# Kernel tuning notes

Measured on AMD Instinct MI355X. Metric: run time of the kernel, lower is better.

## Reference

```python
import jax, jax.numpy as jnp
import numpy as np

RADIUS = 0.1
NSAMPLE = 32


def setup_inputs() -> dict:
    key = jax.random.key(0)
    k1, k2, k3, k4, k5 = jax.random.split(key, 5)
    B, NPOINT, N, C = 4, 2048, 8192, 64
    query_xyz = jax.random.uniform(k1, (B, 3, NPOINT), dtype=jnp.float32)
    support_xyz = jax.random.uniform(k2, (B, 3, N), dtype=jnp.float32)
    query_mask = jax.random.bernoulli(k3, 0.9, (B, NPOINT))
    support_mask = jax.random.bernoulli(k4, 0.9, (B, N))
    features = jax.random.normal(k5, (B, C, N), dtype=jnp.float32)
    return {"query_xyz": query_xyz, "support_xyz": support_xyz,
            "query_mask": query_mask, "support_mask": support_mask,
            "features": features}


def _masked_ordered_ball_query(query_xyz, support_xyz, query_mask, support_mask,
                               radius, nsample):
    # query_xyz: (B,3,npoint), support_xyz: (B,3,N)
    q = query_xyz.transpose(0, 2, 1)    # (B, npoint, 3)
    s = support_xyz.transpose(0, 2, 1)  # (B, N, 3)
    N = s.shape[1]
    # squared pairwise distances via |q|^2 + |s|^2 - 2 q.s  -> (B, npoint, N)
    d2 = (jnp.sum(q * q, -1)[:, :, None]
          + jnp.sum(s * s, -1)[:, None, :]
          - 2.0 * jnp.einsum('bpd,bnd->bpn', q, s))
    within = (d2 <= radius * radius) \
        & support_mask[:, None, :] & query_mask[:, :, None]
    # ordered selection of the first `nsample` in-ball indices (ascending index)
    score = jnp.where(within, N - jnp.arange(N, dtype=jnp.int32), 0)
    vals, idx = jax.lax.top_k(score, nsample)     # (B, npoint, nsample)
    idx_mask = vals > 0                            # true neighbors
    # pad slots with the first found neighbor (0 if none found)
    first = jnp.where(idx_mask[..., :1], idx[..., :1], 0)
    idx = jnp.where(idx_mask, idx, first)
    return idx, idx_mask


def _group(points_nc, idx):
    # points_nc: (B, N, D), idx: (B, npoint, nsample) -> (B, npoint, nsample, D)
    return jax.vmap(lambda p, i: p[i])(points_nc, idx)


def reference(query_xyz, support_xyz, query_mask, support_mask, features):
    idx, idx_mask = _masked_ordered_ball_query(
        query_xyz, support_xyz, query_mask, support_mask, RADIUS, NSAMPLE)
    s = support_xyz.transpose(0, 2, 1)             # (B, N, 3)
    grouped_xyz = _group(s, idx).transpose(0, 3, 1, 2)   # (B,3,npoint,nsample)
    grouped_xyz = grouped_xyz - query_xyz[:, :, :, None]
    grouped_xyz = grouped_xyz / RADIUS             # normalize_xyz=True
    f = features.transpose(0, 2, 1)                # (B, N, C)
    grouped_features = _group(f, idx).transpose(0, 3, 1, 2)  # (B,C,npoint,nsample)
    new_features = jnp.concatenate([grouped_xyz, grouped_features], axis=1)
    return new_features, idx_mask
```

## Files before the change

kernel.cpp:

```cpp
#include <hip/hip_runtime.h>


#define NPOINT 2048
#define NSUP   8192
#define NCH    64
#define NS     32
#define GRID1  10
#define CELLS  1000
#define QCHUNK 1024

__device__ __forceinline__ bool probe_mask4(const void* mask) {
    const unsigned char* mb = (const unsigned char*)mask;
    const int lane = threadIdx.x & 63;
    return __ballot(mb[4 * lane + 1] != 0) == 0ull;
}
__device__ __forceinline__ bool read_mask(const void* mask, int i, bool is4) {
    return is4 ? (((const int*)mask)[i] != 0)
               : (((const unsigned char*)mask)[i] != 0);
}
__device__ __forceinline__ int cell_of(float x, float y, float z) {
    const int cx = min(GRID1 - 1, (int)(x * 10.0f));
    const int cy = min(GRID1 - 1, (int)(y * 10.0f));
    const int cz = min(GRID1 - 1, (int)(z * 10.0f));
    return cx + GRID1 * cy + GRID1 * GRID1 * cz;
}

__global__ __launch_bounds__(1024) void build_grid(
    const float* __restrict__ support_xyz, const void* __restrict__ support_mask,
    int* __restrict__ starts, float4* __restrict__ pts)
{
    __shared__ int hist[CELLS];
    __shared__ int scanb[1024];
    __shared__ int cur[CELLS];
    const int b   = blockIdx.x;
    const int tid = threadIdx.x;
    const bool m4 = probe_mask4(support_mask);
    const float* sx = support_xyz + (size_t)b * 3 * NSUP;

    if (tid < CELLS) { hist[tid] = 0; cur[tid] = 0; }
    __syncthreads();

    float xr[8], yr[8], zr[8]; int cidr[8]; bool mr[8];
    #pragma unroll
    for (int i = 0; i < 8; ++i) {
        const int n = tid + 1024 * i;
        xr[i] = sx[n];
        yr[i] = sx[NSUP + n];
        zr[i] = sx[2 * NSUP + n];
        mr[i] = read_mask(support_mask, b * NSUP + n, m4);
        cidr[i] = cell_of(xr[i], yr[i], zr[i]);
        if (mr[i]) atomicAdd(&hist[cidr[i]], 1);
    }
    __syncthreads();

    scanb[tid] = (tid < CELLS) ? hist[tid] : 0;
    __syncthreads();
    for (int d = 1; d < 1024; d <<= 1) {
        int v = 0;
        if (tid >= d) v = scanb[tid - d];
        __syncthreads();
        if (tid >= d) scanb[tid] += v;
        __syncthreads();
    }
    int* stg = starts + b * (CELLS + 1);
    if (tid == 0) stg[0] = 0;
    if (tid < CELLS) stg[tid + 1] = scanb[tid];

    #pragma unroll
    for (int i = 0; i < 8; ++i) {
        if (mr[i]) {
            const int c    = cidr[i];
            const int base = (c == 0) ? 0 : scanb[c - 1];
            const int pos  = base + atomicAdd(&cur[c], 1);
            pts[(size_t)b * NSUP + pos] =
                make_float4(xr[i], yr[i], zr[i], __int_as_float(tid + 1024 * i));
        }
    }
}

__global__ __launch_bounds__(256) void mqag_query(
    const float* __restrict__ query_xyz, const float* __restrict__ support_xyz,
    const void* __restrict__ query_mask, const void* __restrict__ support_mask,
    const float4* __restrict__ pts, const int* __restrict__ starts,
    int* __restrict__ idx_ws, float* __restrict__ out, int B)
{
#pragma clang fp contract(off)
    const int wib  = threadIdx.x >> 6;
    const int lane = threadIdx.x & 63;
    const int qid  = blockIdx.x * 4 + wib;
    const int b    = qid / NPOINT;
    const int p    = qid % NPOINT;

    __shared__ int hits_all[4][64];
    __shared__ int slots_all[4][NS];
    int* hits  = hits_all[wib];
    int* slots = slots_all[wib];

    const bool m4q = probe_mask4(query_mask);

    const float* sx = support_xyz + (size_t)b * 3 * NSUP;
    const float* sy = sx + NSUP;
    const float* sz = sx + 2 * NSUP;

    const float qx = query_xyz[(size_t)b * 3 * NPOINT + p];
    const float qy = query_xyz[(size_t)b * 3 * NPOINT + NPOINT + p];
    const float qz = query_xyz[(size_t)b * 3 * NPOINT + 2 * NPOINT + p];
    const bool  qm = read_mask(query_mask, b * NPOINT + p, m4q);
    const float qq = (qx * qx + qy * qy) + qz * qz;

    int T = 0;
    int eT[16], aT[16];
    if (qm) {
        const int x0 = max(0, (int)floorf((qx - 0.101f) * 10.f));
        const int x1 = min(GRID1 - 1, (int)floorf((qx + 0.101f) * 10.f));
        const int y0 = max(0, (int)floorf((qy - 0.101f) * 10.f));
        const int y1 = min(GRID1 - 1, (int)floorf((qy + 0.101f) * 10.f));
        const int z0 = max(0, (int)floorf((qz - 0.101f) * 10.f));
        const int z1 = min(GRID1 - 1, (int)floorf((qz + 0.101f) * 10.f));
        const int ncx = x1 - x0 + 1;
        const int* stb = starts + b * (CELLS + 1);

        const int jz = lane >> 2, jy = lane & 3;
        const int cz = z0 + jz,  cy = y0 + jy;
        const bool act = (lane < 16) && (cz <= z1) && (cy <= y1);
        int len = 0, s0 = 0;
        if (act) {
            const int c0 = x0 + GRID1 * cy + GRID1 * GRID1 * cz;
            s0  = stb[c0];
            len = stb[c0 + ncx] - s0;
        }
        int pre = len;
        #pragma unroll
        for (int d = 1; d < 64; d <<= 1) {
            const int v = __shfl_up(pre, d, 64);
            if (lane >= d) pre += v;
        }
        const int adj = s0 - (pre - len);
        #pragma unroll
        for (int j = 0; j < 16; ++j) {
            eT[j] = __builtin_amdgcn_readlane(pre, j);
            aT[j] = __builtin_amdgcn_readlane(adj, j);
        }
        T = eT[15];
    }

    int cnt = 0;
    const float4* ptsb = pts + (size_t)b * NSUP;
    for (int tb = 0; tb < T; tb += 64) {
        const int  g     = tb + lane;
        const bool valid = g < T;
        int adj = 0;
        #pragma unroll
        for (int j = 15; j >= 0; --j)
            if (g < eT[j]) adj = aT[j];
        const float4 pv = ptsb[valid ? (g + adj) : 0];
        const int nidx = __float_as_int(pv.w);
        const float ss  = (pv.x * pv.x + pv.y * pv.y) + pv.z * pv.z;
        const float dot = __builtin_fmaf(qz, pv.z,
                          __builtin_fmaf(qy, pv.y, qx * pv.x));
        const float d2  = (qq + ss) - 2.0f * dot;
        const bool within = valid && (d2 <= 0.01f);
        const unsigned long long bal = __ballot(within);
        if (within) {
            const int r = cnt + __popcll(bal & ((1ull << lane) - 1ull));
            if (r < 64) hits[r] = nidx;
        }
        cnt += __popcll(bal);
    }

    __syncthreads();

    if (cnt > 64) {
        const bool m4s = probe_mask4(support_mask);
        int c2 = 0;
        for (int basei = 0; basei < NSUP; basei += 64) {
            const int n = basei + lane;
            const float x = sx[n], y = sy[n], z = sz[n];
            const bool  m = read_mask(support_mask, b * NSUP + n, m4s);
            const float ss  = (x * x + y * y) + z * z;
            const float dot = __builtin_fmaf(qz, z,
                              __builtin_fmaf(qy, y, qx * x));
            const float d2  = (qq + ss) - 2.0f * dot;
            const bool within = (d2 <= 0.01f) && m;
            const unsigned long long bal = __ballot(within);
            if (within) {
                const int r = c2 + __popcll(bal & ((1ull << lane) - 1ull));
                if (r < NS) slots[r] = n;
            }
            c2 += __popcll(bal);
            if (c2 >= NS) break;
        }
        cnt = c2;
    } else {
        int v = (lane < cnt) ? hits[lane] : 0x7FFFFFFF;
        #pragma unroll
        for (int k = 2; k <= 64; k <<= 1) {
            #pragma unroll
            for (int j = k >> 1; j > 0; j >>= 1) {
                const int pv = __shfl_xor(v, j, 64);
                const bool keep_min = ((lane & j) == 0) == ((lane & k) == 0);
                const int mn = min(v, pv), mx = max(v, pv);
                v = keep_min ? mn : mx;
            }
        }
        if (lane < NS && lane < cnt) slots[lane] = v;
    }
    const int found = (cnt < NS) ? cnt : NS;

    __syncthreads();
    const int first = (found > 0) ? slots[0] : 0;
    if (lane < NS && lane >= found) slots[lane] = first;
    __syncthreads();

    if (lane < NS) idx_ws[((size_t)b * NPOINT + p) * NS + lane] = slots[lane];

    const size_t nf_elems = (size_t)B * 67 * NPOINT * NS;
    if (lane < NS) {
        out[nf_elems + ((size_t)b * NPOINT + p) * NS + lane] =
            (lane < found) ? 1.0f : 0.0f;
    }

    for (int i = 0; i < 2; ++i) {
        const int flat = i * 64 + lane;
        if (flat < 3 * NS) {
            const int ch = flat >> 5;
            const int k  = flat & 31;
            const int idx = slots[k];
            const float s = sx[(size_t)ch * NSUP + idx];
            const float q = (ch == 0) ? qx : ((ch == 1) ? qy : qz);
            out[(((size_t)b * 67 + ch) * NPOINT + p) * NS + k] = (s - q) / 0.1f;
        }
    }
}

__global__ __launch_bounds__(256) void gather_feat(
    const float* __restrict__ features, const int* __restrict__ idx_ws,
    float* __restrict__ out, int B)
{
    __shared__ float row[NSUP];
    const int bc = blockIdx.y;
    const int b  = bc / NCH, ch = bc % NCH;
    const int p0 = blockIdx.x * QCHUNK;

    const float* src = features + ((size_t)b * NCH + ch) * NSUP;
    const float4* src4 = (const float4*)src;
    for (int i = threadIdx.x; i < NSUP / 4; i += 256)
        ((float4*)row)[i] = src4[i];
    __syncthreads();

    const int4* idx4 = (const int4*)(idx_ws + ((size_t)b * NPOINT + p0) * NS);
    float4* dst4 = (float4*)(out + (((size_t)b * 67 + 3 + ch) * NPOINT + p0) * NS);
    for (int e = threadIdx.x; e < QCHUNK * NS / 4; e += 256) {
        const int4 iv = idx4[e];
        dst4[e] = make_float4(row[iv.x], row[iv.y], row[iv.z], row[iv.w]);
    }
}

__global__ __launch_bounds__(256) void mqag_linear(
    const float* __restrict__ query_xyz, const float* __restrict__ support_xyz,
    const void* __restrict__ query_mask_raw, const void* __restrict__ support_mask_raw,
    const float* __restrict__ features, float* __restrict__ out, int B)
{
#pragma clang fp contract(off)
    const int wib  = threadIdx.x >> 6;
    const int lane = threadIdx.x & 63;
    const int qid  = blockIdx.x * 4 + wib;
    const int b    = qid / NPOINT;
    const int p    = qid % NPOINT;

    __shared__ int slots_all[4][NS];
    int* slots = slots_all[wib];

    const bool m4s = probe_mask4(support_mask_raw);
    const bool m4q = probe_mask4(query_mask_raw);

    const float* sx = support_xyz + (size_t)b * 3 * NSUP;
    const float* sy = sx + NSUP;
    const float* sz = sx + 2 * NSUP;

    const float qx = query_xyz[(size_t)b * 3 * NPOINT + p];
    const float qy = query_xyz[(size_t)b * 3 * NPOINT + NPOINT + p];
    const float qz = query_xyz[(size_t)b * 3 * NPOINT + 2 * NPOINT + p];
    const bool  qm = read_mask(query_mask_raw, b * NPOINT + p, m4q);
    const float qq = (qx * qx + qy * qy) + qz * qz;

    int cnt = 0;
    if (qm) {
        for (int base = 0; base < NSUP; base += 64) {
            const int n = base + lane;
            const float x = sx[n], y = sy[n], z = sz[n];
            const bool  m = read_mask(support_mask_raw, b * NSUP + n, m4s);
            const float ss  = (x * x + y * y) + z * z;
            const float dot = __builtin_fmaf(qz, z, __builtin_fmaf(qy, y, qx * x));
            const float d2  = (qq + ss) - 2.0f * dot;
            const bool within = (d2 <= 0.01f) && m;
            const unsigned long long bal = __ballot(within);
            if (within) {
                const int r = cnt + __popcll(bal & ((1ull << lane) - 1ull));
                if (r < NS) slots[r] = n;
            }
            cnt += __popcll(bal);
            if (cnt >= NS) break;
        }
    }
    const int found = cnt < NS ? cnt : NS;
    __syncthreads();
    const int first = (found > 0) ? slots[0] : 0;
    if (lane < NS && lane >= found) slots[lane] = first;
    __syncthreads();

    const size_t nf_elems = (size_t)B * 67 * NPOINT * NS;
    if (lane < NS) {
        out[nf_elems + ((size_t)b * NPOINT + p) * NS + lane] =
            (lane < found) ? 1.0f : 0.0f;
    }
    const float* feat = features + (size_t)b * NCH * NSUP;
    for (int i = 0; i < (67 * NS + 63) / 64; ++i) {
        const int flat = i * 64 + lane;
        if (flat < 67 * NS) {
            const int ch = flat >> 5;
            const int k  = flat & 31;
            const int idx = slots[k];
            float val;
            if (ch < 3) {
                const float s = sx[(size_t)ch * NSUP + idx];
                const float q = (ch == 0) ? qx : ((ch == 1) ? qy : qz);
                val = (s - q) / 0.1f;
            } else {
                val = feat[(size_t)(ch - 3) * NSUP + idx];
            }
            out[(((size_t)b * 67 + ch) * NPOINT + p) * NS + k] = val;
        }
    }
}

extern "C" void kernel_launch(void* const* d_in, const int* in_sizes, int n_in,
                              void* d_out, int out_size, void* d_ws, size_t ws_size,
                              hipStream_t stream) {
    const float* query_xyz    = (const float*)d_in[0];
    const float* support_xyz  = (const float*)d_in[1];
    const void*  query_mask   = d_in[2];
    const void*  support_mask = d_in[3];
    const float* features     = (const float*)d_in[4];

    const int B = in_sizes[0] / (3 * NPOINT);

    const size_t off_pts    = 0;
    const size_t off_starts = off_pts + (size_t)B * NSUP * sizeof(float4);
    const size_t off_idx    = off_starts + (size_t)B * (CELLS + 1) * sizeof(int);
    const size_t need = off_idx + (size_t)B * NPOINT * NS * sizeof(int);

    if (ws_size >= need) {
        float4* pts  = (float4*)((char*)d_ws + off_pts);
        int* starts  = (int*)((char*)d_ws + off_starts);
        int* idx_ws  = (int*)((char*)d_ws + off_idx);

        hipLaunchKernelGGL(build_grid, dim3(B), dim3(1024), 0, stream,
                           support_xyz, support_mask, starts, pts);
        hipLaunchKernelGGL(mqag_query, dim3(B * NPOINT / 4), dim3(256), 0,
                           stream, query_xyz, support_xyz, query_mask,
                           support_mask, pts, starts, idx_ws, (float*)d_out, B);
        hipLaunchKernelGGL(gather_feat, dim3(NPOINT / QCHUNK, B * NCH), dim3(256),
                           0, stream, features, idx_ws, (float*)d_out, B);
    } else {
        hipLaunchKernelGGL(mqag_linear, dim3(B * NPOINT / 4), dim3(256), 0,
                           stream, query_xyz, support_xyz, query_mask,
                           support_mask, features, (float*)d_out, B);
    }
}
```

Measured before the change: 116.6 us.

## Prune grid cells by sphere bounds, prefetch candidates, replace block scan with wave scan

```diff
diff --git a/kernel.cpp b/kernel.cpp
--- a/kernel.cpp
+++ b/kernel.cpp
@@ -30,10 +30,13 @@
     int* __restrict__ starts, float4* __restrict__ pts)
 {
     __shared__ int hist[CELLS];
-    __shared__ int scanb[1024];
+    __shared__ int scanb[CELLS];
     __shared__ int cur[CELLS];
-    const int b   = blockIdx.x;
-    const int tid = threadIdx.x;
+    __shared__ int wavesum[16];
+    const int b    = blockIdx.x;
+    const int tid  = threadIdx.x;
+    const int wid  = tid >> 6;
+    const int lane = tid & 63;
     const bool m4 = probe_mask4(support_mask);
     const float* sx = support_xyz + (size_t)b * 3 * NSUP;
 
@@ -53,18 +56,29 @@
     }
     __syncthreads();
 
-    scanb[tid] = (tid < CELLS) ? hist[tid] : 0;
-    __syncthreads();
-    for (int d = 1; d < 1024; d <<= 1) {
-        int v = 0;
-        if (tid >= d) v = scanb[tid - d];
-        __syncthreads();
-        if (tid >= d) scanb[tid] += v;
-        __syncthreads();
-    }
+    int v = (tid < CELLS) ? hist[tid] : 0;
+    #pragma unroll
+    for (int d = 1; d < 64; d <<= 1) {
+        const int u = __shfl_up(v, d, 64);
+        if (lane >= d) v += u;
+    }
+    if (lane == 63) wavesum[wid] = v;
+    __syncthreads();
+    if (wid == 0) {
+        int w = (lane < 16) ? wavesum[lane] : 0;
+        #pragma unroll
+        for (int d = 1; d < 16; d <<= 1) {
+            const int u = __shfl_up(w, d, 64);
+            if (lane >= d) w += u;
+        }
+        if (lane < 16) wavesum[lane] = w;
+    }
+    __syncthreads();
+    if (wid > 0) v += wavesum[wid - 1];
     int* stg = starts + b * (CELLS + 1);
     if (tid == 0) stg[0] = 0;
-    if (tid < CELLS) stg[tid + 1] = scanb[tid];
+    if (tid < CELLS) { stg[tid + 1] = v; scanb[tid] = v; }
+    __syncthreads();
 
     #pragma unroll
     for (int i = 0; i < 8; ++i) {
@@ -117,21 +131,32 @@
         const int y1 = min(GRID1 - 1, (int)floorf((qy + 0.101f) * 10.f));
         const int z0 = max(0, (int)floorf((qz - 0.101f) * 10.f));
         const int z1 = min(GRID1 - 1, (int)floorf((qz + 0.101f) * 10.f));
-        const int ncx = x1 - x0 + 1;
         const int* stb = starts + b * (CELLS + 1);
 
         const int jz = lane >> 2, jy = lane & 3;
         const int cz = z0 + jz,  cy = y0 + jy;
-        const bool act = (lane < 16) && (cz <= z1) && (cy <= y1);
+        bool act = (lane < 16) && (cz <= z1) && (cy <= y1);
         int len = 0, s0 = 0;
         if (act) {
-            const int c0 = x0 + GRID1 * cy + GRID1 * GRID1 * cz;
-            s0  = stb[c0];
-            len = stb[c0 + ncx] - s0;
-        }
+            const float cyl = cy * 0.1f, czl = cz * 0.1f;
+            const float dy = fmaxf(0.0f, fmaxf(cyl - qy, qy - (cyl + 0.1f)));
+            const float dz = fmaxf(0.0f, fmaxf(czl - qz, qz - (czl + 0.1f)));
+            const float rem = 0.0101f - (dy * dy + dz * dz);
+            if (rem < 0.0f) {
+                act = false;
+            } else {
+                const float mx = sqrtf(rem);
+                const int x0r = max(x0, (int)floorf((qx - mx - 0.0005f) * 10.f));
+                const int x1r = min(x1, (int)floorf((qx + mx + 0.0005f) * 10.f));
+                const int c0 = x0r + GRID1 * cy + GRID1 * GRID1 * cz;
+                s0  = stb[c0];
+                len = stb[c0 + (x1r - x0r + 1)] - s0;
+            }
+        }
+        if (!act) { len = 0; s0 = 0; }
         int pre = len;
         #pragma unroll
-        for (int d = 1; d < 64; d <<= 1) {
+        for (int d = 1; d < 16; d <<= 1) {
             const int v = __shfl_up(pre, d, 64);
             if (lane >= d) pre += v;
         }
@@ -144,16 +169,25 @@
         T = eT[15];
     }
 
-    int cnt = 0;
     const float4* ptsb = pts + (size_t)b * NSUP;
-    for (int tb = 0; tb < T; tb += 64) {
-        const int  g     = tb + lane;
-        const bool valid = g < T;
-        int adj = 0;
+    auto resolve = [&](int g) {
+        int adjv = 0;
         #pragma unroll
         for (int j = 15; j >= 0; --j)
-            if (g < eT[j]) adj = aT[j];
-        const float4 pv = ptsb[valid ? (g + adj) : 0];
+            if (g < eT[j]) adjv = aT[j];
+        return g + adjv;
+    };
+    int cnt = 0;
+    float4 pv;
+    if (T > 0) pv = ptsb[(lane < T) ? resolve(lane) : 0];
+    for (int tb = 0; tb < T; tb += 64) {
+        float4 nx;
+        const int tb2 = tb + 64;
+        if (tb2 < T) {
+            const int gn = tb2 + lane;
+            nx = ptsb[(gn < T) ? resolve(gn) : 0];
+        }
+        const bool valid = (tb + lane) < T;
         const int nidx = __float_as_int(pv.w);
         const float ss  = (pv.x * pv.x + pv.y * pv.y) + pv.z * pv.z;
         const float dot = __builtin_fmaf(qz, pv.z,
@@ -166,9 +200,8 @@
             if (r < 64) hits[r] = nidx;
         }
         cnt += __popcll(bal);
-    }
-
-    __syncthreads();
+        pv = nx;
+    }
 
     if (cnt > 64) {
         const bool m4s = probe_mask4(support_mask);
@@ -197,9 +230,9 @@
         for (int k = 2; k <= 64; k <<= 1) {
             #pragma unroll
             for (int j = k >> 1; j > 0; j >>= 1) {
-                const int pv = __shfl_xor(v, j, 64);
+                const int pv2 = __shfl_xor(v, j, 64);
                 const bool keep_min = ((lane & j) == 0) == ((lane & k) == 0);
-                const int mn = min(v, pv), mx = max(v, pv);
+                const int mn = min(v, pv2), mx = max(v, pv2);
                 v = keep_min ? mn : mx;
             }
         }
@@ -207,10 +240,8 @@
     }
     const int found = (cnt < NS) ? cnt : NS;
 
-    __syncthreads();
     const int first = (found > 0) ? slots[0] : 0;
     if (lane < NS && lane >= found) slots[lane] = first;
-    __syncthreads();
 
     if (lane < NS) idx_ws[((size_t)b * NPOINT + p) * NS + lane] = slots[lane];
 
```

After: 114.6 us. Within noise of the previous version (-1.8%).
